# Optimization experiments

Measured on AMD Instinct MI355X. Metric: run time of the kernel, lower is better.

The kernel has to match this reference:

```python
import jax, jax.numpy as jnp
import numpy as np

V, E, H, K = 50000, 256, 256, 16   # vocab, embed_dim, bi_lstm_hidden, n_tags (E must equal H)
HD = H // 2                        # per-direction hidden
B, NSEG, S = 32, 8, 128            # batch, segments, segment size
T = NSEG * S


def _lstm_dir(x, mask, Wih, Whh, b, h0, c0, reverse):
    """Masked (packed-equivalent) unidirectional LSTM. x:[T,B,E], mask:[T,B]."""
    def step(carry, inp):
        h, c = carry
        xt, mt = inp
        g = xt @ Wih.T + h @ Whh.T + b
        i, f, gg, o = jnp.split(g, 4, axis=-1)  # torch gate order i,f,g,o
        cn = jax.nn.sigmoid(f) * c + jax.nn.sigmoid(i) * jnp.tanh(gg)
        hn = jax.nn.sigmoid(o) * jnp.tanh(cn)
        m = mt[:, None]
        return (jnp.where(m, hn, h), jnp.where(m, cn, c)), jnp.where(m, hn, 0.0)
    (hT, cT), out = jax.lax.scan(step, (h0, c0), (x, mask), reverse=reverse)
    return out, (hT, cT)


def _bilstm(x, lengths, pf, pb, init=None):
    """pack_padded_sequence-equivalent BiLSTM. x:[T,B,E], lengths:[B]."""
    Tt, Bb = x.shape[0], x.shape[1]
    mask = jnp.arange(Tt)[:, None] < lengths[None, :]
    z = jnp.zeros((Bb, HD), x.dtype)
    h0f, c0f, h0b, c0b = init if init is not None else (z, z, z, z)
    of, (hf, cf) = _lstm_dir(x, mask, pf[0], pf[1], pf[2], h0f, c0f, False)
    ob, (hb, cb) = _lstm_dir(x, mask, pb[0], pb[1], pb[2], h0b, c0b, True)
    return jnp.concatenate([of, ob], -1), (hf, cf, hb, cb)


def _viterbi(emission, mask, start, trans, end):
    """torchcrf-style masked Viterbi decode. emission:[T,B,K], mask:[T,B]."""
    score = start[None, :] + emission[0]  # [B,K]
    def step(sc, inp):
        em, m = inp
        allsc = sc[:, :, None] + trans[None, :, :] + em[:, None, :]  # [B,K,K]
        best = jnp.max(allsc, axis=1)
        idx = jnp.argmax(allsc, axis=1).astype(jnp.int32)
        return jnp.where(m[:, None], best, sc), idx
    final, hist = jax.lax.scan(step, score, (emission[1:], mask[1:]))
    final = final + end[None, :]
    best_score = jnp.max(final, axis=-1)                 # [B]
    last = jnp.argmax(final, axis=-1).astype(jnp.int32)  # [B]
    def back(cur, inp):
        h, m = inp  # h:[B,K] backpointers at step t, m = mask[t+1]
        prev = jnp.take_along_axis(h, cur[:, None], axis=1)[:, 0]
        cur = jnp.where(m, prev, cur)
        return cur, cur
    _, tags_rev = jax.lax.scan(back, last, (hist, mask[1:]), reverse=True)
    tags = jnp.concatenate([tags_rev, last[None]], axis=0)  # [T,B]
    return tags, best_score


def _forward(texts, lengths, emb_table, Wih_f, Whh_f, bih_f, bhh_f,
             Wih_b, Whh_b, bih_b, bhh_b, Wlin, blin,
             crf_start, crf_trans, crf_end):
    pf = (Wih_f, Whh_f, bih_f + bhh_f)
    pb = (Wih_b, Whh_b, bih_b + bhh_b)
    emb = emb_table[texts]                      # [B,NSEG,S,E]
    x = jnp.transpose(emb, (1, 2, 0, 3))        # [NSEG,S,B,E]
    lens_seg = lengths.T                        # [NSEG,B]
    # pass 1: independent BiLSTM per segment (zero init state)
    outs, hids = jax.vmap(lambda xs, ls: _bilstm(xs, ls, pf, pb))(x, lens_seg)
    # positions >= per-segment max length are the raw embeddings (torch.cat with pad_text)
    maxlen = jnp.max(lens_seg, axis=1)          # [NSEG]
    over = jnp.arange(S)[None, :, None] >= maxlen[:, None, None]  # [NSEG,S,1]
    outs = jnp.where(over[..., None], x, outs)  # relies on E == 2*HD == H
    lstm1 = outs.reshape(NSEG * S, B, H)        # torch.cat(outputs, dim=0) -> [T,B,H]
    # get_text_lengths: per sample, valid tokens of all segments first, then pad tokens
    t_idx = jnp.arange(T)
    seg, pos = t_idx // S, t_idx % S
    valid = pos[None, :] < lengths[:, seg]                 # [B,T]
    key2 = jnp.where(valid, t_idx[None, :], t_idx[None, :] + T)
    perm = jnp.argsort(key2, axis=1)                       # [B,T] stable reorder
    lstm1_bt = jnp.transpose(lstm1, (1, 0, 2))             # [B,T,H]
    lstm2_in = jnp.transpose(
        jnp.take_along_axis(lstm1_bt, perm[..., None], axis=1), (1, 0, 2))  # [T,B,H]
    new_len = jnp.sum(lengths, axis=1)                     # [B]
    # pass 2: same LSTM weights, init state = final hidden of LAST segment (self.hidden)
    hf, cf, hb, cb = hids
    init = (hf[-1], cf[-1], hb[-1], cb[-1])
    lstm2_out, _ = _bilstm(lstm2_in, new_len, pf, pb, init)
    emission = lstm2_out @ Wlin.T + blin[None, None, :]    # [T,B,K]
    mask = jnp.arange(T)[:, None] < new_len[None, :]       # [T,B]
    return _viterbi(emission, mask, crf_start, crf_trans, crf_end)


def setup_inputs() -> dict:
    key = jax.random.key(0)
    ks = jax.random.split(key, 16)
    def u(k, shape, n):
        s = 1.0 / np.sqrt(n)
        return jax.random.uniform(k, shape, jnp.float32, -s, s)
    return {
        "texts": jax.random.randint(ks[0], (B, NSEG, S), 0, V).astype(jnp.int32),
        "lengths": jax.random.randint(ks[1], (B, NSEG), 1, S + 1).astype(jnp.int32),
        "emb_table": jax.random.normal(ks[2], (V, E), jnp.float32),
        "Wih_f": u(ks[3], (4 * HD, E), HD), "Whh_f": u(ks[4], (4 * HD, HD), HD),
        "bih_f": u(ks[5], (4 * HD,), HD), "bhh_f": u(ks[6], (4 * HD,), HD),
        "Wih_b": u(ks[7], (4 * HD, E), HD), "Whh_b": u(ks[8], (4 * HD, HD), HD),
        "bih_b": u(ks[9], (4 * HD,), HD), "bhh_b": u(ks[10], (4 * HD,), HD),
        "Wlin": u(ks[11], (K, H), H), "blin": u(ks[12], (K,), H),
        "crf_start": jax.random.uniform(ks[13], (K,), jnp.float32, -0.1, 0.1),
        "crf_trans": jax.random.uniform(ks[14], (K, K), jnp.float32, -0.1, 0.1),
        "crf_end": jax.random.uniform(ks[15], (K,), jnp.float32, -0.1, 0.1),
    }


def reference(texts, lengths, emb_table, Wih_f, Whh_f, bih_f, bhh_f,
              Wih_b, Whh_b, bih_b, bhh_b, Wlin, blin,
              crf_start, crf_trans, crf_end):
    # returns (tags [T,B] int32 padded with last tag beyond each length, viterbi score [B])
    return _forward(texts, lengths, emb_table, Wih_f, Whh_f, bih_f, bhh_f,
                    Wih_b, Whh_b, bih_b, bhh_b, Wlin, blin,
                    crf_start, crf_trans, crf_end)
```

## Files before the change

kernel.cpp:

```cpp
#include <hip/hip_runtime.h>
#include <cstdint>
#include <cstddef>


#define B_    32
#define NSEG_ 8
#define S_    128
#define T_    1024
#define E_    256
#define HD_   128
#define G_    512
#define K_    16
#define KS_   8

#define PIN4(v) asm volatile("" : "+v"((v).x), "+v"((v).y), "+v"((v).z), "+v"((v).w))

#define BAR_LDS() do {                                        \
    asm volatile("s_waitcnt lgkmcnt(0)" ::: "memory");        \
    __builtin_amdgcn_s_barrier();                             \
    __builtin_amdgcn_sched_barrier(0);                        \
} while (0)

__global__ void prep_kernel(const int* __restrict__ lengths,
                            int* __restrict__ seg_off, int* __restrict__ new_len,
                            int* __restrict__ order1,
                            const float* __restrict__ bih_f, const float* __restrict__ bhh_f,
                            const float* __restrict__ bih_b, const float* __restrict__ bhh_b,
                            float* __restrict__ bias1,
                            const float* __restrict__ Wih_f, const float* __restrict__ Wih_b,
                            float* __restrict__ WT1)
{
    __shared__ int s_len[256];
    __shared__ int s_ord[256];
    int gtid = blockIdx.x * blockDim.x + threadIdx.x;
    if (gtid < B_) {
        int acc = 0;
        for (int s = 0; s < NSEG_; s++) { seg_off[gtid*NSEG_ + s] = acc; acc += lengths[gtid*NSEG_ + s]; }
        new_len[gtid] = acc;
    }
    if (gtid < 1024) {
        int n = gtid, dir = n >> 9, j = (n >> 2) & 127, g = n & 3;
        int row = g*128 + j;
        bias1[n] = dir ? (bih_b[row] + bhh_b[row]) : (bih_f[row] + bhh_f[row]);
    }
    if (blockIdx.x == 0) {
        int t = threadIdx.x;
        s_len[t] = lengths[t];
        __syncthreads();
        int my = s_len[t], rank = 0;
        for (int u = 0; u < 256; u++) {
            int lu = s_len[u];
            if (lu > my || (lu == my && u < t)) rank++;
        }
        s_ord[rank] = t;
        __syncthreads();
        order1[t] = s_ord[t];
    }
    for (int e = gtid; e < 256*1024; e += gridDim.x * blockDim.x) {
        int k = e >> 10, n = e & 1023;
        int dir = n >> 9, j = (n >> 2) & 127, g = n & 3;
        int row = g*128 + j;
        WT1[e] = dir ? Wih_b[row*E_ + k] : Wih_f[row*E_ + k];
    }
}

template <int MODE>
__global__ void __launch_bounds__(256, 2)
proj_kernel(const int* __restrict__ texts, const float* __restrict__ emb,
            const float* __restrict__ WT1, const float* __restrict__ bias1,
            const float* __restrict__ lstm_packed, float* __restrict__ xproj,
            const int* __restrict__ seg_off, const int* __restrict__ new_len)
{
    int b  = blockIdx.z;
    int nl = new_len[b];
    int p0 = blockIdx.x * 32;
    if (p0 >= nl) return;
    int j0 = blockIdx.y * 512;

    __shared__ __align__(16) float As[32][256];
    __shared__ const float* rowp[32];
    int tid = threadIdx.x;
    if (tid < 32) {
        int p = p0 + tid;
        const float* r = emb;
        if (p < nl) {
            if (MODE == 0) {
                int sg = 0;
                #pragma unroll
                for (int q = 1; q < NSEG_; q++) if (seg_off[b*NSEG_ + q] <= p) sg = q;
                int t   = p - seg_off[b*NSEG_ + sg];
                int tok = texts[(b*NSEG_ + sg)*S_ + t];
                r = emb + (size_t)tok * E_;
            } else {
                r = lstm_packed + ((size_t)b*T_ + p) * 256;
            }
        }
        rowp[tid] = r;
    }
    __syncthreads();
    #pragma unroll 4
    for (int i = 0; i < 32; i++) As[i][tid] = rowp[i][tid];
    __syncthreads();

    int pg = tid >> 6;
    int jg = tid & 63;
    int j  = j0 + jg*8;
    float acc[8][8];
    #pragma unroll
    for (int i = 0; i < 8; i++)
        #pragma unroll
        for (int c = 0; c < 8; c++) acc[i][c] = 0.f;

    const float* wbase = WT1 + j;
    for (int k = 0; k < 256; k += 4) {
        float4 w00 = *(const float4*)(wbase + (size_t)(k+0)*1024);
        float4 w01 = *(const float4*)(wbase + (size_t)(k+0)*1024 + 4);
        float4 w10 = *(const float4*)(wbase + (size_t)(k+1)*1024);
        float4 w11 = *(const float4*)(wbase + (size_t)(k+1)*1024 + 4);
        float4 w20 = *(const float4*)(wbase + (size_t)(k+2)*1024);
        float4 w21 = *(const float4*)(wbase + (size_t)(k+2)*1024 + 4);
        float4 w30 = *(const float4*)(wbase + (size_t)(k+3)*1024);
        float4 w31 = *(const float4*)(wbase + (size_t)(k+3)*1024 + 4);
        #pragma unroll
        for (int i = 0; i < 8; i++) {
            float4 a = *(const float4*)&As[pg*8 + i][k];
            acc[i][0] = fmaf(a.w, w30.x, fmaf(a.z, w20.x, fmaf(a.y, w10.x, fmaf(a.x, w00.x, acc[i][0]))));
            acc[i][1] = fmaf(a.w, w30.y, fmaf(a.z, w20.y, fmaf(a.y, w10.y, fmaf(a.x, w00.y, acc[i][1]))));
            acc[i][2] = fmaf(a.w, w30.z, fmaf(a.z, w20.z, fmaf(a.y, w10.z, fmaf(a.x, w00.z, acc[i][2]))));
            acc[i][3] = fmaf(a.w, w30.w, fmaf(a.z, w20.w, fmaf(a.y, w10.w, fmaf(a.x, w00.w, acc[i][3]))));
            acc[i][4] = fmaf(a.w, w31.x, fmaf(a.z, w21.x, fmaf(a.y, w11.x, fmaf(a.x, w01.x, acc[i][4]))));
            acc[i][5] = fmaf(a.w, w31.y, fmaf(a.z, w21.y, fmaf(a.y, w11.y, fmaf(a.x, w01.y, acc[i][5]))));
            acc[i][6] = fmaf(a.w, w31.z, fmaf(a.z, w21.z, fmaf(a.y, w11.z, fmaf(a.x, w01.z, acc[i][6]))));
            acc[i][7] = fmaf(a.w, w31.w, fmaf(a.z, w21.w, fmaf(a.y, w11.w, fmaf(a.x, w01.w, acc[i][7]))));
        }
    }
    float4 bs0 = *(const float4*)(bias1 + j);
    float4 bs1 = *(const float4*)(bias1 + j + 4);
    #pragma unroll
    for (int i = 0; i < 8; i++) {
        int p = p0 + pg*8 + i;
        if (p < nl) {
            float4 r0, r1;
            r0.x = acc[i][0] + bs0.x; r0.y = acc[i][1] + bs0.y;
            r0.z = acc[i][2] + bs0.z; r0.w = acc[i][3] + bs0.w;
            r1.x = acc[i][4] + bs1.x; r1.y = acc[i][5] + bs1.y;
            r1.z = acc[i][6] + bs1.z; r1.w = acc[i][7] + bs1.w;
            float* dst = xproj + (((size_t)b*T_ + p) << 10) + j;
            *(float4*)dst       = r0;
            *(float4*)(dst + 4) = r1;
        }
    }
}

__device__ __forceinline__ float sig_f(float x) { return 1.0f / (1.0f + __expf(-x)); }
__device__ __forceinline__ float tanh_f(float x) {
    float xc = fminf(fmaxf(x, -15.0f), 15.0f);
    float e  = __expf(-2.0f * xc);
    return (1.0f - e) / (1.0f + e);
}

__device__ __forceinline__ void lstm_chain(
    const float* __restrict__ Whh,
    const float* __restrict__ xp,
    float* __restrict__ outp,
    int p_base, int len, int dir, int rev,
    const float* __restrict__ h0, const float* __restrict__ c0,
    float* __restrict__ hT, float* __restrict__ cT)
{
    __shared__ __align__(16) float  h_sh[HD_];
    __shared__ __align__(16) float4 psum[4*HD_];
    int t = threadIdx.x;
    int j = t & 127, q = t >> 7;

    float4 w[4][8];
    #pragma unroll
    for (int g = 0; g < 4; g++) {
        const float4* wr = (const float4*)(Whh + (size_t)(j + 128*g) * HD_ + 32*q);
        #pragma unroll
        for (int i = 0; i < 8; i++) { w[g][i] = wr[i]; PIN4(w[g][i]); }
    }

    float c_reg = 0.0f;
    if (t < HD_) {
        h_sh[t] = h0 ? h0[t] : 0.0f;
        c_reg   = c0 ? c0[t] : 0.0f;
    }
    __syncthreads();

    const float4* xcol4 = (const float4*)(xp + (size_t)dir * G_) + j;
    const int     oco   = dir * HD_ + j;

    float4 xv[KS_];
    float  hbuf[KS_];

    for (int gs = 0; gs < len; gs += KS_) {
        if (t < HD_) {
            if (gs > 0) {
                #pragma unroll
                for (int u = 0; u < KS_; u++) {
                    int s = gs - KS_ + u;
                    int p = p_base + (rev ? (len - 1 - s) : s);
                    outp[(size_t)p * 256 + oco] = hbuf[u];
                }
            }
            #pragma unroll
            for (int u = 0; u < KS_; u++) {
                int s = gs + u;
                if (s < len) {
                    int p = p_base + (rev ? (len - 1 - s) : s);
                    xv[u] = xcol4[(size_t)p << 8];
                }
            }
        }
        #pragma unroll
        for (int u = 0; u < KS_; u++) {
            if (gs + u < len) {
                const float4* hv = (const float4*)h_sh + q * 8;
                float4 a0 = make_float4(0.f,0.f,0.f,0.f);
                float4 a1 = a0, a2 = a0, a3 = a0;
                #pragma unroll
                for (int i = 0; i < 8; i++) {
                    float4 h4 = hv[i];
                    a0.x = fmaf(h4.x, w[0][i].x, a0.x); a0.y = fmaf(h4.y, w[0][i].y, a0.y);
                    a0.z = fmaf(h4.z, w[0][i].z, a0.z); a0.w = fmaf(h4.w, w[0][i].w, a0.w);
                    a1.x = fmaf(h4.x, w[1][i].x, a1.x); a1.y = fmaf(h4.y, w[1][i].y, a1.y);
                    a1.z = fmaf(h4.z, w[1][i].z, a1.z); a1.w = fmaf(h4.w, w[1][i].w, a1.w);
                    a2.x = fmaf(h4.x, w[2][i].x, a2.x); a2.y = fmaf(h4.y, w[2][i].y, a2.y);
                    a2.z = fmaf(h4.z, w[2][i].z, a2.z); a2.w = fmaf(h4.w, w[2][i].w, a2.w);
                    a3.x = fmaf(h4.x, w[3][i].x, a3.x); a3.y = fmaf(h4.y, w[3][i].y, a3.y);
                    a3.z = fmaf(h4.z, w[3][i].z, a3.z); a3.w = fmaf(h4.w, w[3][i].w, a3.w);
                }
                psum[q*128 + j] = make_float4((a0.x+a0.y)+(a0.z+a0.w),
                                              (a1.x+a1.y)+(a1.z+a1.w),
                                              (a2.x+a2.y)+(a2.z+a2.w),
                                              (a3.x+a3.y)+(a3.z+a3.w));
                BAR_LDS();
                if (t < HD_) {
                    float4 p0 = psum[j], p1 = psum[128 + j], p2 = psum[256 + j], p3 = psum[384 + j];
                    float gi = xv[u].x + ((p0.x + p1.x) + (p2.x + p3.x));
                    float gf = xv[u].y + ((p0.y + p1.y) + (p2.y + p3.y));
                    float gg = xv[u].z + ((p0.z + p1.z) + (p2.z + p3.z));
                    float go = xv[u].w + ((p0.w + p1.w) + (p2.w + p3.w));
                    float cn = sig_f(gf) * c_reg + sig_f(gi) * tanh_f(gg);
                    c_reg = cn;
                    float hn = sig_f(go) * tanh_f(cn);
                    h_sh[j] = hn;
                    hbuf[u] = hn;
                }
                BAR_LDS();
            }
        }
    }
    if (t < HD_ && len > 0) {
        int gs = ((len - 1) / KS_) * KS_;
        #pragma unroll
        for (int u = 0; u < KS_; u++) {
            int s = gs + u;
            if (s < len) {
                int p = p_base + (rev ? (len - 1 - s) : s);
                outp[(size_t)p * 256 + oco] = hbuf[u];
            }
        }
    }
    if (hT != nullptr && t < HD_) { hT[t] = h_sh[t]; cT[t] = c_reg; }
}

__global__ void __launch_bounds__(512, 1)
lstm1_kernel(const int* __restrict__ lengths, const int* __restrict__ seg_off,
             const int* __restrict__ order1,
             const float* __restrict__ Whh_f, const float* __restrict__ Whh_b,
             const float* __restrict__ xproj, float* __restrict__ lstm_packed,
             float* __restrict__ hinit, float* __restrict__ cinit)
{
    int k = blockIdx.x;
    #pragma unroll
    for (int half = 0; half < 2; half++) {
        int u   = half ? (511 - k) : k;
        int r   = u >> 1, dir = u & 1;
        int pr  = order1[r];
        int b   = pr >> 3, seg = pr & 7;
        int len = lengths[b*NSEG_ + seg];
        int pb  = seg_off[b*NSEG_ + seg];
        const float* Whh = dir ? Whh_b : Whh_f;
        float* hT = nullptr; float* cT = nullptr;
        if (seg == NSEG_ - 1) {
            hT = hinit + (dir*B_ + b)*HD_;
            cT = cinit + (dir*B_ + b)*HD_;
        }
        lstm_chain(Whh, xproj + ((size_t)b << 20), lstm_packed + (size_t)b*T_*256,
                   pb, len, dir, dir, nullptr, nullptr, hT, cT);
    }
}

__global__ void __launch_bounds__(512, 1)
lstm2_kernel(const int* __restrict__ new_len,
             const float* __restrict__ Whh_f, const float* __restrict__ Whh_b,
             const float* __restrict__ xproj, float* __restrict__ lstm_packed,
             const float* __restrict__ hinit, const float* __restrict__ cinit)
{
    int cid = blockIdx.x;
    int b = cid >> 1, dir = cid & 1;
    int len = new_len[b];
    const float* Whh = dir ? Whh_b : Whh_f;
    lstm_chain(Whh, xproj + ((size_t)b << 20), lstm_packed + (size_t)b*T_*256,
               0, len, dir, dir,
               hinit + (dir*B_ + b)*HD_, cinit + (dir*B_ + b)*HD_,
               nullptr, nullptr);
}

__global__ void __launch_bounds__(256)
emission_kernel(const float* __restrict__ lstm_packed, const float* __restrict__ Wlin,
                const float* __restrict__ blin, float* __restrict__ emis,
                const int* __restrict__ new_len)
{
    int b  = blockIdx.y;
    int nl = new_len[b];
    int p0 = blockIdx.x * 16;
    if (p0 >= nl) return;
    int pl = threadIdx.x >> 4, s = threadIdx.x & 15;
    int p  = p0 + pl;
    const float4* xr = (const float4*)(lstm_packed + ((size_t)b*T_ + p) * 256);
    const float4* wr = (const float4*)(Wlin + (size_t)s * 256);
    float ax = 0.f, ay = 0.f, az = 0.f, aw = 0.f;
    #pragma unroll
    for (int i = 0; i < 64; i++) {
        float4 a = xr[i]; float4 ww = wr[i];
        ax = fmaf(a.x, ww.x, ax); ay = fmaf(a.y, ww.y, ay);
        az = fmaf(a.z, ww.z, az); aw = fmaf(a.w, ww.w, aw);
    }
    if (p < nl) emis[((size_t)b*T_ + p)*K_ + s] = (ax + ay) + (az + aw) + blin[s];
}

__global__ void __launch_bounds__(64)
viterbi_kernel(const float* __restrict__ emis, const float* __restrict__ start,
               const float* __restrict__ trans, const float* __restrict__ endv,
               const int* __restrict__ new_len, float* __restrict__ out)
{
    int b    = blockIdx.x;
    int nl   = new_len[b];
    int lane = threadIdx.x;
    int s    = lane & 15, q4 = lane >> 4;

    __shared__ unsigned char hist[T_ * K_];
    __shared__ unsigned char tagb[T_];

    float tr[4];
    #pragma unroll
    for (int jj = 0; jj < 4; jj++) tr[jj] = trans[(q4*4 + jj)*K_ + s];

    const float* em = emis + (size_t)b * T_ * K_;
    float sc = start[s] + em[s];

    for (int p = 1; p < nl; p++) {
        float e = em[p*K_ + s];
        float m = -3.4e38f; int a = 0;
        #pragma unroll
        for (int jj = 0; jj < 4; jj++) {
            int q   = q4*4 + jj;
            float sq = __shfl(sc, q, 16);
            float v  = sq + tr[jj];
            if (v > m) { m = v; a = q; }
        }
        #pragma unroll
        for (int d = 16; d < 64; d <<= 1) {
            float mo = __shfl_xor(m, d);
            int   ao = __shfl_xor(a, d);
            if (mo > m || (mo == m && ao < a)) { m = mo; a = ao; }
        }
        sc = m + e;
        if (lane < K_) hist[p*K_ + s] = (unsigned char)a;
    }

    float m = sc + endv[s]; int a = s;
    #pragma unroll
    for (int d = 1; d < 16; d <<= 1) {
        float mo = __shfl_xor(m, d);
        int   ao = __shfl_xor(a, d);
        if (mo > m || (mo == m && ao < a)) { m = mo; a = ao; }
    }
    int last = a;
    if (lane == 0) out[T_*B_ + b] = m;
    __syncthreads();

    for (int i = lane; i < T_; i += 64) tagb[i] = (unsigned char)last;
    __syncthreads();
    if (lane == 0) {
        int cur = last;
        for (int j = nl - 2; j >= 0; j--) {
            cur = hist[(j+1)*K_ + cur];
            tagb[j] = (unsigned char)cur;
        }
    }
    __syncthreads();
    for (int i = lane; i < T_; i += 64) out[(size_t)i*B_ + b] = (float)tagb[i];
}

extern "C" void kernel_launch(void* const* d_in, const int* in_sizes, int n_in,
                              void* d_out, int out_size, void* d_ws, size_t ws_size,
                              hipStream_t stream)
{
    (void)in_sizes; (void)n_in; (void)out_size; (void)ws_size;
    const int*   texts   = (const int*)  d_in[0];
    const int*   lengths = (const int*)  d_in[1];
    const float* emb     = (const float*)d_in[2];
    const float* Wih_f   = (const float*)d_in[3];
    const float* Whh_f   = (const float*)d_in[4];
    const float* bih_f   = (const float*)d_in[5];
    const float* bhh_f   = (const float*)d_in[6];
    const float* Wih_b   = (const float*)d_in[7];
    const float* Whh_b   = (const float*)d_in[8];
    const float* bih_b   = (const float*)d_in[9];
    const float* bhh_b   = (const float*)d_in[10];
    const float* Wlin    = (const float*)d_in[11];
    const float* blin    = (const float*)d_in[12];
    const float* c_start = (const float*)d_in[13];
    const float* c_trans = (const float*)d_in[14];
    const float* c_end   = (const float*)d_in[15];
    float* out = (float*)d_out;

    char* w = (char*)d_ws;
    int*   seg_off     = (int*)(w);
    int*   new_len     = (int*)(w + 1024);
    int*   order1      = (int*)(w + 2048);
    float* bias1       = (float*)(w + 4096);
    float* WT1         = (float*)(w + 8192);
    float* hinit       = (float*)(w + 8192 + 1048576);
    float* cinit       = hinit + 8192;
    float* lstm_packed = cinit + 8192;
    float* xproj       = lstm_packed + (size_t)B_*T_*256;
    float* emis        = xproj + ((size_t)B_ << 20);

    prep_kernel<<<128, 256, 0, stream>>>(lengths, seg_off, new_len, order1,
                                         bih_f, bhh_f, bih_b, bhh_b, bias1,
                                         Wih_f, Wih_b, WT1);
    proj_kernel<0><<<dim3(32, 2, B_), 256, 0, stream>>>(texts, emb, WT1, bias1,
                                                        lstm_packed, xproj, seg_off, new_len);
    lstm1_kernel<<<256, 512, 0, stream>>>(lengths, seg_off, order1, Whh_f, Whh_b,
                                          xproj, lstm_packed, hinit, cinit);
    proj_kernel<1><<<dim3(32, 2, B_), 256, 0, stream>>>(texts, emb, WT1, bias1,
                                                        lstm_packed, xproj, seg_off, new_len);
    lstm2_kernel<<<64, 512, 0, stream>>>(new_len, Whh_f, Whh_b,
                                         xproj, lstm_packed, hinit, cinit);
    emission_kernel<<<dim3(64, B_), 256, 0, stream>>>(lstm_packed, Wlin, blin, emis, new_len);
    viterbi_kernel<<<B_, 64, 0, stream>>>(emis, c_start, c_trans, c_end, new_len, out);
}
```

Baseline: 1.552 ms.

## Double-buffer LSTM input loads and output stores; prefetch Viterbi emissions

Splits the 8-step LSTM recurrence block into two 4-step halves with ping-pong buffers, so the input projection loads for one half and the hidden-state stores for the other are issued while the previous half computes. This is meant to hide global memory latency on the serial recurrence critical path. The Viterbi loop also prefetches the next step's emission value one iteration ahead. The cost is more live registers and more complex tail handling of the output writes.

```diff
diff --git a/kernel.cpp b/kernel.cpp
--- a/kernel.cpp
+++ b/kernel.cpp
@@ -11,7 +11,6 @@
 #define HD_   128
 #define G_    512
 #define K_    16
-#define KS_   8
 
 #define PIN4(v) asm volatile("" : "+v"((v).x), "+v"((v).y), "+v"((v).z), "+v"((v).w))
 
@@ -159,6 +158,42 @@
     return (1.0f - e) / (1.0f + e);
 }
 
+#define LSTM_STEP(XU, HB) do {                                                      \
+    const float4* hv = (const float4*)h_sh + q * 8;                                 \
+    float4 a0 = make_float4(0.f,0.f,0.f,0.f);                                       \
+    float4 a1 = a0, a2 = a0, a3 = a0;                                               \
+    _Pragma("unroll")                                                               \
+    for (int i = 0; i < 8; i++) {                                                   \
+        float4 h4 = hv[i];                                                          \
+        a0.x = fmaf(h4.x, w[0][i].x, a0.x); a0.y = fmaf(h4.y, w[0][i].y, a0.y);     \
+        a0.z = fmaf(h4.z, w[0][i].z, a0.z); a0.w = fmaf(h4.w, w[0][i].w, a0.w);     \
+        a1.x = fmaf(h4.x, w[1][i].x, a1.x); a1.y = fmaf(h4.y, w[1][i].y, a1.y);     \
+        a1.z = fmaf(h4.z, w[1][i].z, a1.z); a1.w = fmaf(h4.w, w[1][i].w, a1.w);     \
+        a2.x = fmaf(h4.x, w[2][i].x, a2.x); a2.y = fmaf(h4.y, w[2][i].y, a2.y);     \
+        a2.z = fmaf(h4.z, w[2][i].z, a2.z); a2.w = fmaf(h4.w, w[2][i].w, a2.w);     \
+        a3.x = fmaf(h4.x, w[3][i].x, a3.x); a3.y = fmaf(h4.y, w[3][i].y, a3.y);     \
+        a3.z = fmaf(h4.z, w[3][i].z, a3.z); a3.w = fmaf(h4.w, w[3][i].w, a3.w);     \
+    }                                                                               \
+    psum[q*128 + j] = make_float4((a0.x+a0.y)+(a0.z+a0.w),                          \
+                                  (a1.x+a1.y)+(a1.z+a1.w),                          \
+                                  (a2.x+a2.y)+(a2.z+a2.w),                          \
+                                  (a3.x+a3.y)+(a3.z+a3.w));                         \
+    BAR_LDS();                                                                      \
+    if (t < HD_) {                                                                  \
+        float4 p0 = psum[j], p1 = psum[128 + j], p2 = psum[256 + j], p3 = psum[384 + j]; \
+        float gi = (XU).x + ((p0.x + p1.x) + (p2.x + p3.x));                        \
+        float gf = (XU).y + ((p0.y + p1.y) + (p2.y + p3.y));                        \
+        float gg = (XU).z + ((p0.z + p1.z) + (p2.z + p3.z));                        \
+        float go = (XU).w + ((p0.w + p1.w) + (p2.w + p3.w));                        \
+        float cn = sig_f(gf) * c_reg + sig_f(gi) * tanh_f(gg);                      \
+        c_reg = cn;                                                                 \
+        float hn = sig_f(go) * tanh_f(cn);                                          \
+        h_sh[j] = hn;                                                               \
+        (HB) = hn;                                                                  \
+    }                                                                               \
+    BAR_LDS();                                                                      \
+} while (0)
+
 __device__ __forceinline__ void lstm_chain(
     const float* __restrict__ Whh,
     const float* __restrict__ xp,
@@ -185,80 +220,67 @@
         h_sh[t] = h0 ? h0[t] : 0.0f;
         c_reg   = c0 ? c0[t] : 0.0f;
     }
-    __syncthreads();
 
     const float4* xcol4 = (const float4*)(xp + (size_t)dir * G_) + j;
     const int     oco   = dir * HD_ + j;
 
-    float4 xv[KS_];
-    float  hbuf[KS_];
-
-    for (int gs = 0; gs < len; gs += KS_) {
+    float4 xvA[4], xvB[4];
+    float  hbufA[4], hbufB[4];
+
+    if (t < HD_) {
+        #pragma unroll
+        for (int u = 0; u < 4; u++)
+            if (u < len) xvA[u] = xcol4[(size_t)(p_base + (rev ? (len-1-u) : u)) << 8];
+    }
+    __syncthreads();
+
+    for (int gs = 0; gs < len; gs += 8) {
         if (t < HD_) {
             if (gs > 0) {
                 #pragma unroll
-                for (int u = 0; u < KS_; u++) {
-                    int s = gs - KS_ + u;
+                for (int u = 0; u < 4; u++) {
+                    int s = gs - 4 + u;
                     int p = p_base + (rev ? (len - 1 - s) : s);
-                    outp[(size_t)p * 256 + oco] = hbuf[u];
+                    outp[(size_t)p * 256 + oco] = hbufB[u];
                 }
             }
             #pragma unroll
-            for (int u = 0; u < KS_; u++) {
+            for (int u = 0; u < 4; u++) {
+                int s = gs + 4 + u;
+                if (s < len) xvB[u] = xcol4[(size_t)(p_base + (rev ? (len-1-s) : s)) << 8];
+            }
+        }
+        #pragma unroll
+        for (int u = 0; u < 4; u++)
+            if (gs + u < len) LSTM_STEP(xvA[u], hbufA[u]);
+
+        if (t < HD_) {
+            #pragma unroll
+            for (int u = 0; u < 4; u++) {
                 int s = gs + u;
                 if (s < len) {
                     int p = p_base + (rev ? (len - 1 - s) : s);
-                    xv[u] = xcol4[(size_t)p << 8];
+                    outp[(size_t)p * 256 + oco] = hbufA[u];
                 }
             }
-        }
-        #pragma unroll
-        for (int u = 0; u < KS_; u++) {
-            if (gs + u < len) {
-                const float4* hv = (const float4*)h_sh + q * 8;
-                float4 a0 = make_float4(0.f,0.f,0.f,0.f);
-                float4 a1 = a0, a2 = a0, a3 = a0;
-                #pragma unroll
-                for (int i = 0; i < 8; i++) {
-                    float4 h4 = hv[i];
-                    a0.x = fmaf(h4.x, w[0][i].x, a0.x); a0.y = fmaf(h4.y, w[0][i].y, a0.y);
-                    a0.z = fmaf(h4.z, w[0][i].z, a0.z); a0.w = fmaf(h4.w, w[0][i].w, a0.w);
-                    a1.x = fmaf(h4.x, w[1][i].x, a1.x); a1.y = fmaf(h4.y, w[1][i].y, a1.y);
-                    a1.z = fmaf(h4.z, w[1][i].z, a1.z); a1.w = fmaf(h4.w, w[1][i].w, a1.w);
-                    a2.x = fmaf(h4.x, w[2][i].x, a2.x); a2.y = fmaf(h4.y, w[2][i].y, a2.y);
-                    a2.z = fmaf(h4.z, w[2][i].z, a2.z); a2.w = fmaf(h4.w, w[2][i].w, a2.w);
-                    a3.x = fmaf(h4.x, w[3][i].x, a3.x); a3.y = fmaf(h4.y, w[3][i].y, a3.y);
-                    a3.z = fmaf(h4.z, w[3][i].z, a3.z); a3.w = fmaf(h4.w, w[3][i].w, a3.w);
-                }
-                psum[q*128 + j] = make_float4((a0.x+a0.y)+(a0.z+a0.w),
-                                              (a1.x+a1.y)+(a1.z+a1.w),
-                                              (a2.x+a2.y)+(a2.z+a2.w),
-                                              (a3.x+a3.y)+(a3.z+a3.w));
-                BAR_LDS();
-                if (t < HD_) {
-                    float4 p0 = psum[j], p1 = psum[128 + j], p2 = psum[256 + j], p3 = psum[384 + j];
-                    float gi = xv[u].x + ((p0.x + p1.x) + (p2.x + p3.x));
-                    float gf = xv[u].y + ((p0.y + p1.y) + (p2.y + p3.y));
-                    float gg = xv[u].z + ((p0.z + p1.z) + (p2.z + p3.z));
-                    float go = xv[u].w + ((p0.w + p1.w) + (p2.w + p3.w));
-                    float cn = sig_f(gf) * c_reg + sig_f(gi) * tanh_f(gg);
-                    c_reg = cn;
-                    float hn = sig_f(go) * tanh_f(cn);
-                    h_sh[j] = hn;
-                    hbuf[u] = hn;
-                }
-                BAR_LDS();
-            }
-        }
+            #pragma unroll
+            for (int u = 0; u < 4; u++) {
+                int s = gs + 8 + u;
+                if (s < len) xvA[u] = xcol4[(size_t)(p_base + (rev ? (len-1-s) : s)) << 8];
+            }
+        }
+        #pragma unroll
+        for (int u = 0; u < 4; u++)
+            if (gs + 4 + u < len) LSTM_STEP(xvB[u], hbufB[u]);
     }
     if (t < HD_ && len > 0) {
-        int gs = ((len - 1) / KS_) * KS_;
-        #pragma unroll
-        for (int u = 0; u < KS_; u++) {
-            int s = gs + u;
+        int lastgs = ((len - 1) / 8) * 8;
+        #pragma unroll
+        for (int u = 0; u < 4; u++) {
+            int s = lastgs + 4 + u;
             if (s < len) {
                 int p = p_base + (rev ? (len - 1 - s) : s);
-                outp[(size_t)p * 256 + oco] = hbuf[u];
+                outp[(size_t)p * 256 + oco] = hbufB[u];
             }
         }
     }
@@ -351,8 +373,10 @@
     const float* em = emis + (size_t)b * T_ * K_;
     float sc = start[s] + em[s];
 
+    float e_next = (nl > 1) ? em[K_ + s] : 0.f;
     for (int p = 1; p < nl; p++) {
-        float e = em[p*K_ + s];
+        float e = e_next;
+        if (p + 1 < nl) e_next = em[(p+1)*K_ + s];
         float m = -3.4e38f; int a = 0;
         #pragma unroll
         for (int jj = 0; jj < 4; jj++) {
```

New measurement: 1.726 ms. 11.2% more time.
